# Optimization experiments

Hardware: AMD Instinct MI355X
Metric: run time of the kernel (lower is better)

The kernel has to match this reference:

```python
import jax, jax.numpy as jnp
import numpy as np

ROI, P = 28, 7          # ROI window on feature map; output grid 7x7 -> 4x4 bins
BIN = ROI // P
C, CLASSES = 64, 2      # channels after vgg features[:2]; n classes
H = W = 512
N_ROI = 2000
D_FC = 4096


def setup_inputs() -> dict:
    key = jax.random.key(0)
    k = jax.random.split(key, 8)
    s = 0.02
    return {
        "img": jax.random.normal(k[0], (3, H, W), jnp.float32),
        "regions": jax.random.randint(k[1], (N_ROI, 2), 0, H - ROI, jnp.int32),
        "conv_w": jax.random.normal(k[2], (C, 3, 3, 3), jnp.float32) * s,
        "conv_b": jnp.zeros((C,), jnp.float32),
        "fc1_w": jax.random.normal(k[3], (D_FC, C * P * P), jnp.float32) * s,
        "fc1_b": jnp.zeros((D_FC,), jnp.float32),
        "fc2_w": jax.random.normal(k[4], (D_FC, D_FC), jnp.float32) * s,
        "fc2_b": jnp.zeros((D_FC,), jnp.float32),
        "cls_w": jax.random.normal(k[5], (CLASSES, D_FC), jnp.float32) * s,
        "cls_b": jnp.zeros((CLASSES,), jnp.float32),
        "bbox_w": jax.random.normal(k[6], (CLASSES * 4, D_FC), jnp.float32) * s,
        "bbox_b": jnp.zeros((CLASSES * 4,), jnp.float32),
    }


def reference(img, regions, conv_w, conv_b, fc1_w, fc1_b,
              fc2_w, fc2_b, cls_w, cls_b, bbox_w, bbox_b):
    # conv trunk: vgg16.features[:2] = Conv2d(3,64,3,pad=1) + ReLU
    fmap = jax.lax.conv_general_dilated(
        img[None], conv_w, window_strides=(1, 1), padding="SAME",
        dimension_numbers=("NCHW", "OIHW", "NCHW"))[0]
    fmap = jax.nn.relu(fmap + conv_b[:, None, None])        # [C, H, W]

    # per-region crop (irregular gather), vectorized over regions
    def crop(rc):
        return jax.lax.dynamic_slice(fmap, (0, rc[0], rc[1]), (C, ROI, ROI))
    rois = jax.vmap(crop)(regions)                          # [N, C, ROI, ROI]

    # RoI max pooling: divide ROIxROI window into PxP grid, max each bin
    pooled = rois.reshape(N_ROI, C, P, BIN, P, BIN).max(axis=(3, 5))  # [N,C,P,P]
    feat = pooled.reshape(N_ROI, C * P * P)

    # vgg classifier[:-1] (Dropout = identity at inference)
    feat = jax.nn.relu(feat @ fc1_w.T + fc1_b)
    feat = jax.nn.relu(feat @ fc2_w.T + fc2_b)              # [N, 4096]

    cls_logits = feat @ cls_w.T + cls_b                     # [N, CLASSES]
    loc_bbox = feat @ bbox_w.T + bbox_b                     # [N, CLASSES*4]
    return (cls_logits, loc_bbox)
```

## Files before the change

### kernel.cpp

```cpp
#include <hip/hip_runtime.h>

typedef unsigned short u16;
typedef unsigned int u32;
using bf16x8 = __attribute__((ext_vector_type(8))) short;
using f32x4  = __attribute__((ext_vector_type(4))) float;
using ushort8 = __attribute__((ext_vector_type(8))) unsigned short;

__device__ __forceinline__ u16 f2bf(float f) {
  u32 u = __float_as_uint(f);
  return (u16)((u + 0x7FFFu + ((u >> 16) & 1u)) >> 16);
}
__device__ __forceinline__ float bf2f(u16 h) {
  return __uint_as_float(((u32)h) << 16);
}
__device__ __forceinline__ ushort8 umax8(ushort8 a, ushort8 b) {
  return __builtin_elementwise_max(a, b);
}
__device__ __forceinline__ void cvt_chunk(const float* __restrict__ in,
                                          u16* __restrict__ out, int i) {
  float4 v = ((const float4*)in)[i];
  uint2 o;
  o.x = (u32)f2bf(v.x) | ((u32)f2bf(v.y) << 16);
  o.y = (u32)f2bf(v.z) | ((u32)f2bf(v.w) << 16);
  ((uint2*)out)[i] = o;
}

__global__ __launch_bounds__(512) void conv_vmax_k(
    const float* __restrict__ img, const float* __restrict__ w,
    const float* __restrict__ bias, u16* __restrict__ M1,
    const float* __restrict__ w1f, u16* __restrict__ w1b) {
  const int t = threadIdx.x;
  const int bid = blockIdx.x;
  const int r3 = bid % 3, q3 = bid / 3;
  if (r3 == 2) {
    int idx = q3 * 512 + t;
    for (int i = idx; i < 3211264; i += 262144) cvt_chunk(w1f, w1b, i);
    return;
  }
  const int widx = q3 * 2 + r3;
  const int x = ((widx & 15) << 5) + (t >> 4);
  const int cq = (t & 15) << 2;
  const int y0 = (widx >> 4) << 3;

  float wr[27][4];
#pragma unroll
  for (int p = 0; p < 27; ++p)
#pragma unroll
    for (int c = 0; c < 4; ++c) wr[p][c] = w[(cq + c) * 27 + p];
  float bz[4];
#pragma unroll
  for (int c = 0; c < 4; ++c) bz[c] = bias[cq + c];

  const bool xm = (x > 0), xp = (x < 511);
  float win[3][3][3];

#define LOADROW(yy, s)                                                        \
  do {                                                                        \
    if ((yy) >= 0 && (yy) <= 511) {                                          \
      _Pragma("unroll") for (int ci = 0; ci < 3; ++ci) {                      \
        const float* rp = img + ci * 262144 + (yy) * 512 + x;                 \
        win[ci][s][0] = xm ? rp[-1] : 0.f;                                    \
        win[ci][s][1] = rp[0];                                                \
        win[ci][s][2] = xp ? rp[1] : 0.f;                                     \
      }                                                                        \
    } else {                                                                   \
      _Pragma("unroll") for (int ci = 0; ci < 3; ++ci) {                      \
        win[ci][s][0] = 0.f; win[ci][s][1] = 0.f; win[ci][s][2] = 0.f;        \
      }                                                                        \
    }                                                                          \
  } while (0)

  LOADROW(y0 - 1, 0);
  LOADROW(y0, 1);

  float h0[4], h1[4], h2[4], cur[4];
#pragma unroll
  for (int i = 0; i < 11; ++i) {
    const int r = y0 + i;
    LOADROW(r + 1, 2);
    if (r <= 511) {
#pragma unroll
      for (int c = 0; c < 4; ++c) cur[c] = bz[c];
#pragma unroll
      for (int ci = 0; ci < 3; ++ci)
#pragma unroll
        for (int ky = 0; ky < 3; ++ky)
#pragma unroll
          for (int kx = 0; kx < 3; ++kx) {
            const float iv = win[ci][ky][kx];
            const int p = ci * 9 + ky * 3 + kx;
#pragma unroll
            for (int c = 0; c < 4; ++c) cur[c] = fmaf(wr[p][c], iv, cur[c]);
          }
#pragma unroll
      for (int c = 0; c < 4; ++c) cur[c] = fmaxf(cur[c], 0.f);
    } else {
#pragma unroll
      for (int c = 0; c < 4; ++c) cur[c] = 0.f;
    }
    if (i >= 3) {
      const int ym = r - 3;
      float m[4];
#pragma unroll
      for (int c = 0; c < 4; ++c)
        m[c] = fmaxf(fmaxf(h0[c], h1[c]), fmaxf(h2[c], cur[c]));
      uint2 o;
      o.x = (u32)f2bf(m[0]) | ((u32)f2bf(m[1]) << 16);
      o.y = (u32)f2bf(m[2]) | ((u32)f2bf(m[3]) << 16);
      *(uint2*)(M1 + (((size_t)(ym * 512 + x)) << 6) + cq) = o;
    }
#pragma unroll
    for (int c = 0; c < 4; ++c) { h0[c] = h1[c]; h1[c] = h2[c]; h2[c] = cur[c]; }
#pragma unroll
    for (int ci = 0; ci < 3; ++ci)
#pragma unroll
      for (int kx = 0; kx < 3; ++kx) {
        win[ci][0][kx] = win[ci][1][kx];
        win[ci][1][kx] = win[ci][2][kx];
      }
  }
#undef LOADROW
}

__global__ __launch_bounds__(256) void roipool2_k(
    const u16* __restrict__ M1, const int* __restrict__ regions,
    u16* __restrict__ feat, const float* __restrict__ w2f,
    u16* __restrict__ w2b) {
  const int t = threadIdx.x;
  const int bid = blockIdx.x;
  const int r5 = bid % 5, q5 = bid / 5;
  if (r5 == 4) {
    int idx = q5 * 256 + t;
    for (int i = idx; i < 4194304; i += 131072) cvt_chunk(w2f, w2b, i);
    return;
  }
  const int n = q5 * 4 + r5;
  uint4* fdst = (uint4*)(feat + (size_t)n * 3136);
  if (n >= 2000) {
    uint4 z; z.x = z.y = z.z = z.w = 0u;
    for (int w = t; w < 392; w += 256) fdst[w] = z;
    return;
  }
  __shared__ u16 frow[3136];
  int r0 = regions[2 * n], c0 = regions[2 * n + 1];
  for (int w = t; w < 392; w += 256) {
    int bin = w >> 3, cg = w & 7;
    int py = bin / 7, px = bin % 7;
    int y = r0 + py * 4, xb = c0 + px * 4;
    const u16* base = M1 + (((size_t)(y * 512 + xb)) << 6) + cg * 8;
    ushort8 a = *(const ushort8*)(base);
    ushort8 b = *(const ushort8*)(base + 64);
    ushort8 c = *(const ushort8*)(base + 128);
    ushort8 d = *(const ushort8*)(base + 192);
    ushort8 m = umax8(umax8(a, b), umax8(c, d));
#pragma unroll
    for (int k = 0; k < 8; ++k) frow[(cg * 8 + k) * 49 + bin] = m[k];
  }
  __syncthreads();
  const uint4* fsrc = (const uint4*)frow;
  for (int w = t; w < 392; w += 256) fdst[w] = fsrc[w];
}

__global__ __launch_bounds__(512, 2) void gemm8_bt_relu_k(
    const u16* __restrict__ A, const u16* __restrict__ B,
    const float* __restrict__ bias, u16* __restrict__ C, int N, int K) {
  __shared__ uint4 lds4[9216];
  char* ldsb = (char*)lds4;
  const int t = threadIdx.x;
  const int lane = t & 63, wv = t >> 6;
  const int wm = wv >> 2, wn = wv & 3;

  int bid = blockIdx.x;
  int swz = ((bid & 7) << 5) | (bid >> 3);
  const int nb = swz >> 4, mb = swz & 15;
  const int m0 = mb * 128, n0 = nb * 256;

  const u16* __restrict__ Ab = A + (size_t)m0 * K;
  const u16* __restrict__ Bb = B + (size_t)n0 * K;

  const int srow = t >> 3;
  const int sslot = (t & 7) ^ (srow & 7);
  const u16* pA0 = Ab + (size_t)srow * K + sslot * 8;
  const u16* pA1 = pA0 + (size_t)64 * K;
  const u16* pB0 = Bb + (size_t)srow * K + sslot * 8;
  const u16* pB1 = pB0 + (size_t)64 * K;
  const u16* pB2 = pB0 + (size_t)128 * K;
  const u16* pB3 = pB0 + (size_t)192 * K;
  const int dof = t * 16;

#define G2L(src, ldst)                                                        \
  __builtin_amdgcn_global_load_lds(                                          \
      (const __attribute__((address_space(1))) void*)(src),                  \
      (__attribute__((address_space(3))) void*)(ldst), 16, 0, 0)

  const int rA = wm * 64 + (lane & 15);
  const int rB = wn * 64 + (lane & 15);
  const int sl = lane >> 4;
#define LOFF(r, slot) (((r) << 7) + ((((slot) ^ ((r) & 7))) << 4))

  f32x4 acc[4][4] = {};
  bf16x8 afr[4][2], bfr[4][2];

  const int NT = K >> 6;
  {
    char* A0 = ldsb; char* B0 = A0 + 16384;
    char* A1 = ldsb + 49152; char* B1 = A1 + 16384;
    G2L(pA0, A0 + dof); G2L(pA1, A0 + 8192 + dof);
    G2L(pB0, B0 + dof); G2L(pB1, B0 + 8192 + dof);
    G2L(pB2, B0 + 16384 + dof); G2L(pB3, B0 + 24576 + dof);
    G2L(pA0 + 64, A1 + dof); G2L(pA1 + 64, A1 + 8192 + dof);
    G2L(pB0 + 64, B1 + dof); G2L(pB1 + 64, B1 + 8192 + dof);
    G2L(pB2 + 64, B1 + 16384 + dof); G2L(pB3 + 64, B1 + 24576 + dof);
  }
  asm volatile("s_waitcnt vmcnt(6)" ::: "memory");
  __builtin_amdgcn_s_barrier();

  int cb = 0;
  for (int tt = 0; tt < NT; ++tt) {
    const int pb = (cb + 2 >= 3) ? cb - 1 : cb + 2;
    const bool pf = (tt + 2) < NT;
    char* Acur = ldsb + cb * 49152; char* Bcur = Acur + 16384;
    char* Apf  = ldsb + pb * 49152; char* Bpf  = Apf + 16384;
    const int kof = (tt + 2) << 6;

    if (pf) {
      G2L(pA0 + kof, Apf + dof);
      G2L(pA1 + kof, Apf + 8192 + dof);
      G2L(pB0 + kof, Bpf + dof);
      G2L(pB1 + kof, Bpf + 8192 + dof);
      G2L(pB2 + kof, Bpf + 16384 + dof);
      G2L(pB3 + kof, Bpf + 24576 + dof);
    }
    __builtin_amdgcn_sched_barrier(0);
    __builtin_amdgcn_s_setprio(1);
#pragma unroll
    for (int j = 0; j < 4; ++j) {
      bfr[j][0] = *(const bf16x8*)(Bcur + LOFF(rB + j * 16, sl));
      bfr[j][1] = *(const bf16x8*)(Bcur + LOFF(rB + j * 16, 4 + sl));
    }
#pragma unroll
    for (int i = 0; i < 4; ++i) {
      afr[i][0] = *(const bf16x8*)(Acur + LOFF(rA + i * 16, sl));
      afr[i][1] = *(const bf16x8*)(Acur + LOFF(rA + i * 16, 4 + sl));
    }
#pragma unroll
    for (int i = 0; i < 4; ++i)
#pragma unroll
      for (int j = 0; j < 4; ++j) {
        acc[i][j] = __builtin_amdgcn_mfma_f32_16x16x32_bf16(afr[i][0], bfr[j][0], acc[i][j], 0, 0, 0);
        acc[i][j] = __builtin_amdgcn_mfma_f32_16x16x32_bf16(afr[i][1], bfr[j][1], acc[i][j], 0, 0, 0);
      }
    __builtin_amdgcn_s_setprio(0);
    if (pf) {
      asm volatile("s_waitcnt vmcnt(6)" ::: "memory");
    } else if (tt + 1 < NT) {
      asm volatile("s_waitcnt vmcnt(0)" ::: "memory");
    }
    __builtin_amdgcn_s_barrier();
    cb = (cb == 2) ? 0 : cb + 1;
  }
#undef G2L
#undef LOFF

  float bv[4];
#pragma unroll
  for (int j = 0; j < 4; ++j) bv[j] = bias[n0 + wn * 64 + j * 16 + (lane & 15)];
#pragma unroll
  for (int i = 0; i < 4; ++i)
#pragma unroll
    for (int j = 0; j < 4; ++j) {
      int cg = n0 + wn * 64 + j * 16 + (lane & 15);
#pragma unroll
      for (int r = 0; r < 4; ++r) {
        int rg = m0 + wm * 64 + i * 16 + (lane >> 4) * 4 + r;
        float v = fmaxf(acc[i][j][r] + bv[j], 0.f);
        C[(size_t)rg * N + cg] = f2bf(v);
      }
    }
}

__global__ __launch_bounds__(256) void heads_k(
    const u16* __restrict__ h2, const float* __restrict__ cw,
    const float* __restrict__ cb, const float* __restrict__ bw,
    const float* __restrict__ bb, float* __restrict__ out) {
  __shared__ u16 wl[10][4096];
  __shared__ float red[4][10];
  const int t = threadIdx.x;
  for (int i4 = t; i4 < 10240; i4 += 256) {
    int j = i4 >> 10, k4 = i4 & 1023;
    float4 v = (j < 2) ? ((const float4*)cw)[j * 1024 + k4]
                       : ((const float4*)bw)[(j - 2) * 1024 + k4];
    uint2 o;
    o.x = (u32)f2bf(v.x) | ((u32)f2bf(v.y) << 16);
    o.y = (u32)f2bf(v.z) | ((u32)f2bf(v.w) << 16);
    *(uint2*)(&wl[j][k4 * 4]) = o;
  }
  __syncthreads();
  const int lane = t & 63, wvi = t >> 6;
  const int m0 = blockIdx.x * 8;
  for (int mi = 0; mi < 8; ++mi) {
    const int m = m0 + mi;
    const u16* hrow = h2 + (size_t)m * 4096;
    float p[10];
#pragma unroll
    for (int j = 0; j < 10; ++j) p[j] = 0.f;
#pragma unroll
    for (int h = 0; h < 2; ++h) {
      const int kc = t + h * 256;
      ushort8 hv = ((const ushort8*)hrow)[kc];
      float hf[8];
#pragma unroll
      for (int e = 0; e < 8; ++e) hf[e] = bf2f(hv[e]);
#pragma unroll
      for (int j = 0; j < 10; ++j) {
        ushort8 wv = *(const ushort8*)(&wl[j][kc * 8]);
#pragma unroll
        for (int e = 0; e < 8; ++e) p[j] = fmaf(hf[e], bf2f(wv[e]), p[j]);
      }
    }
#pragma unroll
    for (int j = 0; j < 10; ++j)
#pragma unroll
      for (int off = 32; off > 0; off >>= 1) p[j] += __shfl_down(p[j], off);
    if (lane == 0) {
#pragma unroll
      for (int j = 0; j < 10; ++j) red[wvi][j] = p[j];
    }
    __syncthreads();
    if (t < 10) {
      float s = red[0][t] + red[1][t] + red[2][t] + red[3][t];
      s += (t < 2) ? cb[t] : bb[t - 2];
      if (t < 2) out[m * 2 + t] = s;
      else out[4000 + m * 8 + (t - 2)] = s;
    }
    __syncthreads();
  }
}

extern "C" void kernel_launch(void* const* d_in, const int* in_sizes, int n_in,
                              void* d_out, int out_size, void* d_ws, size_t ws_size,
                              hipStream_t stream) {
  const float* img    = (const float*)d_in[0];
  const int*   regions= (const int*)d_in[1];
  const float* conv_w = (const float*)d_in[2];
  const float* conv_b = (const float*)d_in[3];
  const float* fc1_w  = (const float*)d_in[4];
  const float* fc1_b  = (const float*)d_in[5];
  const float* fc2_w  = (const float*)d_in[6];
  const float* fc2_b  = (const float*)d_in[7];
  const float* cls_w  = (const float*)d_in[8];
  const float* cls_b  = (const float*)d_in[9];
  const float* bbox_w = (const float*)d_in[10];
  const float* bbox_b = (const float*)d_in[11];
  float* out = (float*)d_out;

  char* ws = (char*)d_ws;
  u16* M1   = (u16*)(ws);
  u16* h1   = (u16*)(ws);
  u16* h2   = (u16*)(ws + 16777216);
  u16* feat = (u16*)(ws + 33554432);
  u16* w1b  = (u16*)(ws + 46399488);
  u16* w2b  = (u16*)(ws + 72089600);

  conv_vmax_k<<<1536, 512, 0, stream>>>(img, conv_w, conv_b, M1, fc1_w, w1b);
  roipool2_k<<<2560, 256, 0, stream>>>(M1, regions, feat, fc2_w, w2b);
  gemm8_bt_relu_k<<<256, 512, 0, stream>>>(feat, w1b, fc1_b, h1, 4096, 3136);
  gemm8_bt_relu_k<<<256, 512, 0, stream>>>(h1, w2b, fc2_b, h2, 4096, 4096);
  heads_k<<<250, 256, 0, stream>>>(h2, cls_w, cls_b, bbox_w, bbox_b, out);
}
```

Before: 220.8 us.

## Use 256x256 split-K GEMM tiles with separate reduce/bias/ReLU passes

Replaces the 128x256 fc GEMM tiles with 256x256 tiles at K-step 32 and splits K in two, so the 256 blocks cover the output with higher operand reuse per block. The two partial results are written as bf16 to separate buffers. A new finalize kernel sums them with bias and ReLU for fc1, and the heads kernel fuses that reduction for fc2. This adds extra global traffic for partials and rounds partial sums to bf16, which can reduce accuracy.

```diff
diff --git a/kernel.cpp b/kernel.cpp
--- a/kernel.cpp
+++ b/kernel.cpp
@@ -161,99 +161,89 @@
   for (int w = t; w < 392; w += 256) fdst[w] = fsrc[w];
 }
 
-__global__ __launch_bounds__(512, 2) void gemm8_bt_relu_k(
+__global__ __launch_bounds__(512, 2) void gemm_sk_k(
     const u16* __restrict__ A, const u16* __restrict__ B,
-    const float* __restrict__ bias, u16* __restrict__ C, int N, int K) {
-  __shared__ uint4 lds4[9216];
+    u16* __restrict__ P, int K, int NT0, int NTtot) {
+  __shared__ uint4 lds4[6144];
   char* ldsb = (char*)lds4;
   const int t = threadIdx.x;
   const int lane = t & 63, wv = t >> 6;
   const int wm = wv >> 2, wn = wv & 3;
 
-  int bid = blockIdx.x;
-  int swz = ((bid & 7) << 5) | (bid >> 3);
-  const int nb = swz >> 4, mb = swz & 15;
-  const int m0 = mb * 128, n0 = nb * 256;
+  const int bid = blockIdx.x;
+  const int xcd = bid & 7, q = bid >> 3;
+  const int sk = xcd >> 2;
+  const int mb = q & 7;
+  const int nb = ((xcd & 3) << 2) | (q >> 3);
+  const int m0 = mb * 256, n0 = nb * 256;
+  const int ts = sk ? NT0 : 0;
+  const int NTb = sk ? (NTtot - NT0) : NT0;
 
   const u16* __restrict__ Ab = A + (size_t)m0 * K;
   const u16* __restrict__ Bb = B + (size_t)n0 * K;
-
-  const int srow = t >> 3;
-  const int sslot = (t & 7) ^ (srow & 7);
-  const u16* pA0 = Ab + (size_t)srow * K + sslot * 8;
-  const u16* pA1 = pA0 + (size_t)64 * K;
-  const u16* pB0 = Bb + (size_t)srow * K + sslot * 8;
-  const u16* pB1 = pB0 + (size_t)64 * K;
-  const u16* pB2 = pB0 + (size_t)128 * K;
-  const u16* pB3 = pB0 + (size_t)192 * K;
+  const int srow = t >> 2;
+  const int sslot = (t & 3) ^ ((srow >> 1) & 3);
+  const u16* pA  = Ab + (size_t)srow * K + sslot * 8;
+  const u16* pA2 = pA + (size_t)128 * K;
+  const u16* pB  = Bb + (size_t)srow * K + sslot * 8;
+  const u16* pB2 = pB + (size_t)128 * K;
   const int dof = t * 16;
 
 #define G2L(src, ldst)                                                        \
   __builtin_amdgcn_global_load_lds(                                          \
       (const __attribute__((address_space(1))) void*)(src),                  \
       (__attribute__((address_space(3))) void*)(ldst), 16, 0, 0)
-
-  const int rA = wm * 64 + (lane & 15);
-  const int rB = wn * 64 + (lane & 15);
-  const int sl = lane >> 4;
-#define LOFF(r, slot) (((r) << 7) + ((((slot) ^ ((r) & 7))) << 4))
-
-  f32x4 acc[4][4] = {};
-  bf16x8 afr[4][2], bfr[4][2];
-
-  const int NT = K >> 6;
+#define LOFF(r, s) (((r) << 6) + ((((s) ^ (((r) >> 1) & 3))) << 4))
+
+  const int row16 = lane & 15, sl = lane >> 4;
+  f32x4 acc[8][4] = {};
+  bf16x8 afr[8], bfr[4];
+
   {
-    char* A0 = ldsb; char* B0 = A0 + 16384;
-    char* A1 = ldsb + 49152; char* B1 = A1 + 16384;
-    G2L(pA0, A0 + dof); G2L(pA1, A0 + 8192 + dof);
-    G2L(pB0, B0 + dof); G2L(pB1, B0 + 8192 + dof);
-    G2L(pB2, B0 + 16384 + dof); G2L(pB3, B0 + 24576 + dof);
-    G2L(pA0 + 64, A1 + dof); G2L(pA1 + 64, A1 + 8192 + dof);
-    G2L(pB0 + 64, B1 + dof); G2L(pB1 + 64, B1 + 8192 + dof);
-    G2L(pB2 + 64, B1 + 16384 + dof); G2L(pB3 + 64, B1 + 24576 + dof);
-  }
-  asm volatile("s_waitcnt vmcnt(6)" ::: "memory");
+    const size_t k0 = (size_t)ts * 32;
+    char* b0 = ldsb;
+    G2L(pA + k0, b0 + dof);          G2L(pA2 + k0, b0 + 8192 + dof);
+    G2L(pB + k0, b0 + 16384 + dof);  G2L(pB2 + k0, b0 + 24576 + dof);
+    if (NTb > 1) {
+      char* b1 = ldsb + 32768;
+      G2L(pA + k0 + 32, b1 + dof);          G2L(pA2 + k0 + 32, b1 + 8192 + dof);
+      G2L(pB + k0 + 32, b1 + 16384 + dof);  G2L(pB2 + k0 + 32, b1 + 24576 + dof);
+      asm volatile("s_waitcnt vmcnt(4)" ::: "memory");
+    } else {
+      asm volatile("s_waitcnt vmcnt(0)" ::: "memory");
+    }
+  }
   __builtin_amdgcn_s_barrier();
 
   int cb = 0;
-  for (int tt = 0; tt < NT; ++tt) {
+  for (int tt = 0; tt < NTb; ++tt) {
     const int pb = (cb + 2 >= 3) ? cb - 1 : cb + 2;
-    const bool pf = (tt + 2) < NT;
-    char* Acur = ldsb + cb * 49152; char* Bcur = Acur + 16384;
-    char* Apf  = ldsb + pb * 49152; char* Bpf  = Apf + 16384;
-    const int kof = (tt + 2) << 6;
-
+    const bool pf = (tt + 2) < NTb;
+    char* cbuf = ldsb + cb * 32768;
     if (pf) {
-      G2L(pA0 + kof, Apf + dof);
-      G2L(pA1 + kof, Apf + 8192 + dof);
-      G2L(pB0 + kof, Bpf + dof);
-      G2L(pB1 + kof, Bpf + 8192 + dof);
-      G2L(pB2 + kof, Bpf + 16384 + dof);
-      G2L(pB3 + kof, Bpf + 24576 + dof);
+      char* fbuf = ldsb + pb * 32768;
+      const size_t kof = (size_t)(ts + tt + 2) * 32;
+      G2L(pA + kof, fbuf + dof);          G2L(pA2 + kof, fbuf + 8192 + dof);
+      G2L(pB + kof, fbuf + 16384 + dof);  G2L(pB2 + kof, fbuf + 24576 + dof);
     }
     __builtin_amdgcn_sched_barrier(0);
     __builtin_amdgcn_s_setprio(1);
-#pragma unroll
-    for (int j = 0; j < 4; ++j) {
-      bfr[j][0] = *(const bf16x8*)(Bcur + LOFF(rB + j * 16, sl));
-      bfr[j][1] = *(const bf16x8*)(Bcur + LOFF(rB + j * 16, 4 + sl));
-    }
-#pragma unroll
-    for (int i = 0; i < 4; ++i) {
-      afr[i][0] = *(const bf16x8*)(Acur + LOFF(rA + i * 16, sl));
-      afr[i][1] = *(const bf16x8*)(Acur + LOFF(rA + i * 16, 4 + sl));
-    }
-#pragma unroll
-    for (int i = 0; i < 4; ++i)
-#pragma unroll
-      for (int j = 0; j < 4; ++j) {
-        acc[i][j] = __builtin_amdgcn_mfma_f32_16x16x32_bf16(afr[i][0], bfr[j][0], acc[i][j], 0, 0, 0);
-        acc[i][j] = __builtin_amdgcn_mfma_f32_16x16x32_bf16(afr[i][1], bfr[j][1], acc[i][j], 0, 0, 0);
-      }
+    char* Bc = cbuf + 16384;
+#pragma unroll
+    for (int j = 0; j < 4; ++j)
+      bfr[j] = *(const bf16x8*)(Bc + LOFF(wn * 64 + j * 16 + row16, sl));
+#pragma unroll
+    for (int i = 0; i < 8; ++i)
+      afr[i] = *(const bf16x8*)(cbuf + LOFF(wm * 128 + i * 16 + row16, sl));
+#pragma unroll
+    for (int i = 0; i < 8; ++i)
+#pragma unroll
+      for (int j = 0; j < 4; ++j)
+        acc[i][j] = __builtin_amdgcn_mfma_f32_16x16x32_bf16(afr[i], bfr[j], acc[i][j], 0, 0, 0);
     __builtin_amdgcn_s_setprio(0);
     if (pf) {
-      asm volatile("s_waitcnt vmcnt(6)" ::: "memory");
-    } else if (tt + 1 < NT) {
+      asm volatile("s_waitcnt vmcnt(4)" ::: "memory");
+    } else if (tt + 1 < NTb) {
       asm volatile("s_waitcnt vmcnt(0)" ::: "memory");
     }
     __builtin_amdgcn_s_barrier();
@@ -262,27 +252,48 @@
 #undef G2L
 #undef LOFF
 
-  float bv[4];
-#pragma unroll
-  for (int j = 0; j < 4; ++j) bv[j] = bias[n0 + wn * 64 + j * 16 + (lane & 15)];
-#pragma unroll
-  for (int i = 0; i < 4; ++i)
+  u16* Pb = P + (size_t)sk * 8388608;
+#pragma unroll
+  for (int i = 0; i < 8; ++i)
 #pragma unroll
     for (int j = 0; j < 4; ++j) {
-      int cg = n0 + wn * 64 + j * 16 + (lane & 15);
+      const int cg = n0 + wn * 64 + j * 16 + row16;
 #pragma unroll
       for (int r = 0; r < 4; ++r) {
-        int rg = m0 + wm * 64 + i * 16 + (lane >> 4) * 4 + r;
-        float v = fmaxf(acc[i][j][r] + bv[j], 0.f);
-        C[(size_t)rg * N + cg] = f2bf(v);
+        const int rg = m0 + wm * 128 + i * 16 + sl * 4 + r;
+        Pb[(size_t)rg * 4096 + cg] = f2bf(acc[i][j][r]);
       }
     }
 }
 
-__global__ __launch_bounds__(256) void heads_k(
-    const u16* __restrict__ h2, const float* __restrict__ cw,
-    const float* __restrict__ cb, const float* __restrict__ bw,
-    const float* __restrict__ bb, float* __restrict__ out) {
+__global__ __launch_bounds__(256) void finalize1_k(
+    const u16* __restrict__ P, const float* __restrict__ bias,
+    u16* __restrict__ H) {
+  int c = blockIdx.x * 256 + threadIdx.x;
+  int row = c >> 9, c8 = (c & 511) << 3;
+  size_t off = (size_t)row * 4096 + c8;
+  ushort8 a = *(const ushort8*)(P + off);
+  ushort8 b = *(const ushort8*)(P + 8388608 + off);
+  float4 b0 = *(const float4*)(bias + c8);
+  float4 b1 = *(const float4*)(bias + c8 + 4);
+  float v[8];
+#pragma unroll
+  for (int e = 0; e < 8; ++e) v[e] = bf2f(a[e]) + bf2f(b[e]);
+  v[0] += b0.x; v[1] += b0.y; v[2] += b0.z; v[3] += b0.w;
+  v[4] += b1.x; v[5] += b1.y; v[6] += b1.z; v[7] += b1.w;
+  uint4 o;
+  o.x = (u32)f2bf(fmaxf(v[0], 0.f)) | ((u32)f2bf(fmaxf(v[1], 0.f)) << 16);
+  o.y = (u32)f2bf(fmaxf(v[2], 0.f)) | ((u32)f2bf(fmaxf(v[3], 0.f)) << 16);
+  o.z = (u32)f2bf(fmaxf(v[4], 0.f)) | ((u32)f2bf(fmaxf(v[5], 0.f)) << 16);
+  o.w = (u32)f2bf(fmaxf(v[6], 0.f)) | ((u32)f2bf(fmaxf(v[7], 0.f)) << 16);
+  *(uint4*)(H + off) = o;
+}
+
+__global__ __launch_bounds__(256) void heads2_k(
+    const u16* __restrict__ P, const float* __restrict__ bias,
+    const float* __restrict__ cw, const float* __restrict__ cb,
+    const float* __restrict__ bw, const float* __restrict__ bb,
+    float* __restrict__ out) {
   __shared__ u16 wl[10][4096];
   __shared__ float red[4][10];
   const int t = threadIdx.x;
@@ -300,20 +311,31 @@
   const int m0 = blockIdx.x * 8;
   for (int mi = 0; mi < 8; ++mi) {
     const int m = m0 + mi;
-    const u16* hrow = h2 + (size_t)m * 4096;
+    if (m >= 2000) break;
+    const size_t roff = (size_t)m * 4096;
     float p[10];
 #pragma unroll
     for (int j = 0; j < 10; ++j) p[j] = 0.f;
 #pragma unroll
     for (int h = 0; h < 2; ++h) {
       const int kc = t + h * 256;
-      ushort8 hv = ((const ushort8*)hrow)[kc];
+      const int c8 = kc * 8;
+      ushort8 a = *(const ushort8*)(P + roff + c8);
+      ushort8 b2 = *(const ushort8*)(P + 8388608 + roff + c8);
+      float4 bi0 = *(const float4*)(bias + c8);
+      float4 bi1 = *(const float4*)(bias + c8 + 4);
       float hf[8];
-#pragma unroll
-      for (int e = 0; e < 8; ++e) hf[e] = bf2f(hv[e]);
+      hf[0] = fmaxf(bf2f(a[0]) + bf2f(b2[0]) + bi0.x, 0.f);
+      hf[1] = fmaxf(bf2f(a[1]) + bf2f(b2[1]) + bi0.y, 0.f);
+      hf[2] = fmaxf(bf2f(a[2]) + bf2f(b2[2]) + bi0.z, 0.f);
+      hf[3] = fmaxf(bf2f(a[3]) + bf2f(b2[3]) + bi0.w, 0.f);
+      hf[4] = fmaxf(bf2f(a[4]) + bf2f(b2[4]) + bi1.x, 0.f);
+      hf[5] = fmaxf(bf2f(a[5]) + bf2f(b2[5]) + bi1.y, 0.f);
+      hf[6] = fmaxf(bf2f(a[6]) + bf2f(b2[6]) + bi1.z, 0.f);
+      hf[7] = fmaxf(bf2f(a[7]) + bf2f(b2[7]) + bi1.w, 0.f);
 #pragma unroll
       for (int j = 0; j < 10; ++j) {
-        ushort8 wv = *(const ushort8*)(&wl[j][kc * 8]);
+        ushort8 wv = *(const ushort8*)(&wl[j][c8]);
 #pragma unroll
         for (int e = 0; e < 8; ++e) p[j] = fmaf(hf[e], bf2f(wv[e]), p[j]);
       }
@@ -356,15 +378,16 @@
 
   char* ws = (char*)d_ws;
   u16* M1   = (u16*)(ws);
-  u16* h1   = (u16*)(ws);
-  u16* h2   = (u16*)(ws + 16777216);
+  u16* P    = (u16*)(ws);
   u16* feat = (u16*)(ws + 33554432);
   u16* w1b  = (u16*)(ws + 46399488);
+  u16* h1   = (u16*)(ws + 46399488);
   u16* w2b  = (u16*)(ws + 72089600);
 
   conv_vmax_k<<<1536, 512, 0, stream>>>(img, conv_w, conv_b, M1, fc1_w, w1b);
   roipool2_k<<<2560, 256, 0, stream>>>(M1, regions, feat, fc2_w, w2b);
-  gemm8_bt_relu_k<<<256, 512, 0, stream>>>(feat, w1b, fc1_b, h1, 4096, 3136);
-  gemm8_bt_relu_k<<<256, 512, 0, stream>>>(h1, w2b, fc2_b, h2, 4096, 4096);
-  heads_k<<<250, 256, 0, stream>>>(h2, cls_w, cls_b, bbox_w, bbox_b, out);
-}
+  gemm_sk_k<<<256, 512, 0, stream>>>(feat, w1b, P, 3136, 49, 98);
+  finalize1_k<<<4096, 256, 0, stream>>>(P, fc1_b, h1);
+  gemm_sk_k<<<256, 512, 0, stream>>>(h1, w2b, P, 4096, 64, 128);
+  heads2_k<<<250, 256, 0, stream>>>(P, fc2_b, cls_w, cls_b, bbox_w, bbox_b, out);
+}
```

Result: slower. 230.8 us (+4.5%).
